# Kernel optimization log

Hardware: AMD Instinct MI355X
Metric: run time of the kernel (lower is better)

The kernel has to match this reference:

```python
import jax, jax.numpy as jnp
import numpy as np

B, N = 2, 512
CS, CZ = 384, 128
H, D, P, PV = 12, 16, 4, 8
W_C = (2.0 / (9.0 * P)) ** 0.5
W_L = (1.0 / 3.0) ** 0.5
CAT = H * CZ + H * D + H * PV * 3 + H * PV  # concat width into output linear


def setup_inputs() -> dict:
    key = jax.random.key(0)
    ks = jax.random.split(key, 14)
    sc = lambda n: np.float32(1.0 / np.sqrt(n))
    s_i = jax.random.normal(ks[0], (B, N, CS), jnp.float32)
    z_ij = jax.random.normal(ks[1], (B, N, N, CZ), jnp.float32)
    rots = jax.random.normal(ks[2], (B, N, 3, 3), jnp.float32)
    trans = jax.random.normal(ks[3], (B, N, 3), jnp.float32)
    wq = jax.random.normal(ks[4], (CS, H, D), jnp.float32) * sc(CS)
    wk = jax.random.normal(ks[5], (CS, H, D), jnp.float32) * sc(CS)
    wv = jax.random.normal(ks[6], (CS, H, D), jnp.float32) * sc(CS)
    wqp = jax.random.normal(ks[7], (CS, H, P, 3), jnp.float32) * sc(CS)
    wkp = jax.random.normal(ks[8], (CS, H, P, 3), jnp.float32) * sc(CS)
    wvp = jax.random.normal(ks[9], (CS, H, PV, 3), jnp.float32) * sc(CS)
    wb = jax.random.normal(ks[10], (CZ, H), jnp.float32) * sc(CZ)
    gamma = jax.random.normal(ks[11], (H,), jnp.float32)
    wout = jax.random.normal(ks[12], (CAT, CS), jnp.float32) * sc(CAT)
    bout = jnp.zeros((CS,), jnp.float32)
    return dict(s_i=s_i, z_ij=z_ij, rots=rots, trans=trans, wq=wq, wk=wk, wv=wv,
                wqp=wqp, wkp=wkp, wvp=wvp, wb=wb, gamma=gamma, wout=wout, bout=bout)


def reference(s_i, z_ij, rots, trans, wq, wk, wv, wqp, wkp, wvp, wb, gamma, wout, bout):
    # rigid apply: x_global = R @ x_local + t, per residue, broadcast over (h, p)
    def rig_apply(x):  # x: (b,i,h,p,3)
        return jnp.einsum('bixy,bihpy->bihpx', rots, x) + trans[:, :, None, None, :]

    def rig_invert_apply(x):  # R^T @ (x - t)
        return jnp.einsum('biyx,bihpy->bihpx', rots, x - trans[:, :, None, None, :])

    q = jnp.einsum('bic,chd->bihd', s_i, wq)
    k = jnp.einsum('bic,chd->bihd', s_i, wk)
    v = jnp.einsum('bic,chd->bihd', s_i, wv)
    qp = jnp.einsum('bic,chpx->bihpx', s_i, wqp)
    kp = jnp.einsum('bic,chpx->bihpx', s_i, wkp)
    vp = jnp.einsum('bic,chpx->bihpx', s_i, wvp)

    b_ij = jnp.einsum('bijc,ch->bijh', z_ij, wb)  # pair bias

    tq = rig_apply(qp)  # (b,i,h,p,3) in global frame
    tk = rig_apply(kp)
    # squared point distances summed over points: (b,i,j,h)
    d2 = jnp.sum((tq[:, :, None] - tk[:, None]) ** 2, axis=(-1, -2))

    a_s = jnp.einsum('bihd,bjhd->bijh', q, k) * np.float32(1.0 / np.sqrt(D))
    logits = W_L * (a_s + b_ij - (W_C * 0.5) * gamma * d2)
    a = jax.nn.softmax(logits, axis=2)  # softmax over j (dim=-2 of bijh)

    o_hat = jnp.einsum('bijh,bijd->bihd', a, z_ij)   # pair-value aggregation
    o = jnp.einsum('bijh,bjhd->bihd', a, v)          # scalar values
    tv = rig_apply(vp)                               # point values in global frame
    o_hp = rig_invert_apply(jnp.einsum('bijh,bjhpx->bihpx', a, tv))
    o_hp_norm = jnp.sqrt(jnp.sum(o_hp ** 2, axis=-1))  # (b,i,h,p)

    cat = jnp.concatenate([
        o_hat.reshape(B, N, H * CZ),
        o.reshape(B, N, H * D),
        o_hp.reshape(B, N, H * PV * 3),
        o_hp_norm.reshape(B, N, H * PV),
    ], axis=-1)
    return cat @ wout + bout
```

## Files before the change

### kernel.cpp

```cpp
#include <hip/hip_runtime.h>
#include <hip/hip_bf16.h>
#include <math.h>

#define BB 2
#define NN 512
#define CS 384
#define CZ 128
#define HH 12
#define CATW 2112

#define W_L_CONST 0.57735026919f
#define W_C_HALF 0.11785113019f
#define INV_SQRT_D 0.25f
#define LGP 516

__global__ void k_proj(const float* __restrict__ s_i,
                       const float* __restrict__ rots,
                       const float* __restrict__ trans,
                       const float* __restrict__ wq,
                       const float* __restrict__ wk,
                       const float* __restrict__ wv,
                       const float* __restrict__ wqp,
                       const float* __restrict__ wkp,
                       const float* __restrict__ wvp,
                       float* __restrict__ qw, float* __restrict__ kw,
                       float* __restrict__ vw, float* __restrict__ tqw,
                       float* __restrict__ tkw, float* __restrict__ tvw) {
  int t0 = blockIdx.x * 2;
  __shared__ float s_row[2][CS];
  __shared__ float praw[2][576];
  __shared__ float R[2][9], T[2][3];
  int tid = threadIdx.x;
  for (int idx = tid; idx < 2 * CS; idx += 256) {
    int tok = idx / CS, c = idx % CS;
    s_row[tok][c] = s_i[(size_t)(t0 + tok) * CS + c];
  }
  if (tid < 18) R[tid / 9][tid % 9] = rots[t0 * 9 + tid];
  if (tid < 6) T[tid / 3][tid % 3] = trans[t0 * 3 + tid];
  __syncthreads();

  for (int f = tid; f < 1152; f += 256) {
    const float* wp;
    int stride;
    if (f < 576) {
      int sel = f / 192, r = f % 192;
      wp = ((sel == 0) ? wq : (sel == 1) ? wk : wv) + r;
      stride = 192;
    } else {
      int g = f - 576;
      if (g < 144)      { wp = wqp + g;        stride = 144; }
      else if (g < 288) { wp = wkp + (g - 144); stride = 144; }
      else              { wp = wvp + (g - 288); stride = 288; }
    }
    float a0 = 0.f, a1 = 0.f;
    #pragma unroll 8
    for (int c = 0; c < CS; c++) {
      float w = wp[(size_t)c * stride];
      a0 += s_row[0][c] * w;
      a1 += s_row[1][c] * w;
    }
    if (f < 576) {
      int sel = f / 192, r = f % 192;
      float* dst = (sel == 0) ? qw : (sel == 1) ? kw : vw;
      dst[(size_t)(t0 + 0) * 192 + r] = a0;
      dst[(size_t)(t0 + 1) * 192 + r] = a1;
    } else {
      int g = f - 576;
      praw[0][g] = a0;
      praw[1][g] = a1;
    }
  }
  __syncthreads();
  for (int idx = tid; idx < 1152; idx += 256) {
    int tok = idx / 576, f = idx % 576;
    int base, r;
    float* dst;
    if (f < 144)      { r = f;       base = 0;   dst = tqw + (size_t)(t0 + tok) * 144; }
    else if (f < 288) { r = f - 144; base = 144; dst = tkw + (size_t)(t0 + tok) * 144; }
    else              { r = f - 288; base = 288; dst = tvw + (size_t)(t0 + tok) * 288; }
    int hp = r / 3, x = r % 3;
    float v0 = praw[tok][base + hp * 3 + 0];
    float v1 = praw[tok][base + hp * 3 + 1];
    float v2 = praw[tok][base + hp * 3 + 2];
    dst[r] = R[tok][x * 3 + 0] * v0 + R[tok][x * 3 + 1] * v1 + R[tok][x * 3 + 2] * v2 + T[tok][x];
  }
}

__global__ void k_bias(const float* __restrict__ z,
                       const float* __restrict__ wb,
                       float* __restrict__ bw) {
  __shared__ float zt[64][129];
  __shared__ float wbs[CZ * HH];
  __shared__ float bbs[64][12];
  int tid = threadIdx.x;
  int r0 = blockIdx.x * 64;
  int bi = r0 >> 9, j0 = r0 & 511;

  for (int idx = tid; idx < CZ * HH; idx += 256) wbs[idx] = wb[idx];
  const float* zbase = z + (size_t)r0 * CZ;
  for (int s = 0; s < 8; s++) {
    int idx = tid + s * 256;
    int row = idx >> 5, q = idx & 31;
    float4 v = *(const float4*)(zbase + (size_t)row * CZ + q * 4);
    zt[row][q * 4 + 0] = v.x;
    zt[row][q * 4 + 1] = v.y;
    zt[row][q * 4 + 2] = v.z;
    zt[row][q * 4 + 3] = v.w;
  }
  __syncthreads();

  int row = tid & 63, hbase = tid >> 6;
  float a0 = 0.f, a1 = 0.f, a2 = 0.f;
  #pragma unroll 8
  for (int c = 0; c < CZ; c++) {
    float zv = zt[row][c];
    a0 += zv * wbs[c * HH + hbase];
    a1 += zv * wbs[c * HH + hbase + 4];
    a2 += zv * wbs[c * HH + hbase + 8];
  }
  bbs[row][hbase] = a0;
  bbs[row][hbase + 4] = a1;
  bbs[row][hbase + 8] = a2;
  __syncthreads();

  for (int idx = tid; idx < 768; idx += 256) {
    int h = idx / 64, jl = idx % 64;
    bw[((size_t)bi * HH + h) * NN + j0 + jl] = bbs[jl][h];
  }
}

__global__ void k_att(const float* __restrict__ z,
                      const float* __restrict__ qw,
                      const float* __restrict__ kw,
                      const float* __restrict__ tqw,
                      const float* __restrict__ tkw,
                      const float* __restrict__ vw,
                      const float* __restrict__ tvw,
                      const float* __restrict__ gamma,
                      const float* __restrict__ rots,
                      const float* __restrict__ trans,
                      const float* __restrict__ bw,
                      float* __restrict__ catm) {
  int bi = blockIdx.x;
  int b = bi / NN;
  __shared__ float lg[HH][LGP];
  __shared__ float opart[4][480];
  __shared__ float qrow[192], tqrow[144], gam[HH];
  __shared__ float rm[HH][4], rs[HH][4];
  __shared__ float praw[288], ohp[288], R[9], T[3];
  int tid = threadIdx.x;
  int lane = tid & 63, wid = tid >> 6;

  const float* bwrow = bw + (size_t)bi * (HH * NN);
  for (int idx = tid; idx < HH * NN; idx += 256)
    lg[idx >> 9][idx & 511] = bwrow[idx];
  for (int idx = tid; idx < 192; idx += 256) qrow[idx] = qw[(size_t)bi * 192 + idx];
  if (tid < 144) tqrow[tid] = tqw[(size_t)bi * 144 + tid];
  if (tid < HH) gam[tid] = gamma[tid];
  if (tid < 9) R[tid] = rots[bi * 9 + tid];
  if (tid < 3) T[tid] = trans[bi * 3 + tid];
  __syncthreads();

  for (int s = 0; s < 24; s++) {
    int task = tid + s * 256;
    int j = task / 12, h = task % 12;
    const float4* kd = (const float4*)(kw + ((size_t)(b * NN + j)) * 192 + h * 16);
    float as = 0.f;
    #pragma unroll
    for (int q = 0; q < 4; q++) {
      float4 kv = kd[q];
      as += qrow[h * 16 + q * 4 + 0] * kv.x + qrow[h * 16 + q * 4 + 1] * kv.y +
            qrow[h * 16 + q * 4 + 2] * kv.z + qrow[h * 16 + q * 4 + 3] * kv.w;
    }
    const float4* td = (const float4*)(tkw + ((size_t)(b * NN + j)) * 144 + h * 12);
    float d2 = 0.f;
    #pragma unroll
    for (int q = 0; q < 3; q++) {
      float4 tv = td[q];
      float d0 = tqrow[h * 12 + q * 4 + 0] - tv.x;
      float d1 = tqrow[h * 12 + q * 4 + 1] - tv.y;
      float d2_ = tqrow[h * 12 + q * 4 + 2] - tv.z;
      float d3 = tqrow[h * 12 + q * 4 + 3] - tv.w;
      d2 += d0 * d0 + d1 * d1 + d2_ * d2_ + d3 * d3;
    }
    lg[h][j] = W_L_CONST * (as * INV_SQRT_D + lg[h][j] - W_C_HALF * gam[h] * d2);
  }
  __syncthreads();

  #pragma unroll
  for (int h = 0; h < HH; h++) {
    float m = fmaxf(lg[h][tid], lg[h][tid + 256]);
    #pragma unroll
    for (int off = 32; off >= 1; off >>= 1) m = fmaxf(m, __shfl_xor(m, off, 64));
    if (lane == 0) rm[h][wid] = m;
  }
  __syncthreads();
  #pragma unroll
  for (int h = 0; h < HH; h++) {
    float mx = fmaxf(fmaxf(rm[h][0], rm[h][1]), fmaxf(rm[h][2], rm[h][3]));
    float e0 = __expf(lg[h][tid] - mx);
    float e1 = __expf(lg[h][tid + 256] - mx);
    lg[h][tid] = e0;
    lg[h][tid + 256] = e1;
    float s = e0 + e1;
    #pragma unroll
    for (int off = 32; off >= 1; off >>= 1) s += __shfl_xor(s, off, 64);
    if (lane == 0) rs[h][wid] = s;
  }
  __syncthreads();
  #pragma unroll
  for (int h = 0; h < HH; h++) {
    float inv = 1.0f / (rs[h][0] + rs[h][1] + rs[h][2] + rs[h][3]);
    lg[h][tid] *= inv;
    lg[h][tid + 256] *= inv;
  }
  __syncthreads();

  float* crow = catm + (size_t)bi * CATW;
  int j0 = wid * 128;

  for (int t = lane; t < 480; t += 64) {
    const float* src;
    int h, str;
    if (t < 192) { h = t >> 4; src = vw + (size_t)b * NN * 192 + t; str = 192; }
    else { int f = t - 192; h = f / 24; src = tvw + (size_t)b * NN * 288 + f; str = 288; }
    float sum = 0.f;
    for (int jj = 0; jj < 128; jj += 4) {
      float4 av = *(const float4*)&lg[h][j0 + jj];
      sum += av.x * src[(size_t)(j0 + jj + 0) * str]
           + av.y * src[(size_t)(j0 + jj + 1) * str]
           + av.z * src[(size_t)(j0 + jj + 2) * str]
           + av.w * src[(size_t)(j0 + jj + 3) * str];
    }
    opart[wid][t] = sum;
  }
  __syncthreads();
  for (int t = tid; t < 480; t += 256) {
    float s = opart[0][t] + opart[1][t] + opart[2][t] + opart[3][t];
    if (t < 192) crow[1536 + t] = s;
    else praw[t - 192] = s;
  }
  __syncthreads();
  for (int f = tid; f < 288; f += 256) {
    int g = f / 3, x = f % 3;
    float v0 = praw[g * 3 + 0] - T[0];
    float v1 = praw[g * 3 + 1] - T[1];
    float v2 = praw[g * 3 + 2] - T[2];
    float val = R[0 * 3 + x] * v0 + R[1 * 3 + x] * v1 + R[2 * 3 + x] * v2;
    ohp[f] = val;
    crow[1728 + f] = val;
  }
  __syncthreads();
  if (tid < 96) {
    float x0 = ohp[tid * 3 + 0];
    float x1 = ohp[tid * 3 + 1];
    float x2 = ohp[tid * 3 + 2];
    crow[2016 + tid] = sqrtf(x0 * x0 + x1 * x1 + x2 * x2);
  }

  int hw = lane >> 5, c4 = (lane & 31) * 4;
  float4 acc[HH];
  #pragma unroll
  for (int h = 0; h < HH; h++) acc[h] = make_float4(0.f, 0.f, 0.f, 0.f);
  for (int stp = 0; stp < 64; stp++) {
    int j = j0 + stp * 2 + hw;
    float4 zv = *(const float4*)(z + ((size_t)bi * NN + j) * CZ + c4);
    #pragma unroll
    for (int h = 0; h < HH; h++) {
      float a = lg[h][j];
      acc[h].x += a * zv.x;
      acc[h].y += a * zv.y;
      acc[h].z += a * zv.z;
      acc[h].w += a * zv.w;
    }
  }
  __syncthreads();
  #pragma unroll
  for (int h = 0; h < HH; h++) {
    acc[h].x += __shfl_xor(acc[h].x, 32, 64);
    acc[h].y += __shfl_xor(acc[h].y, 32, 64);
    acc[h].z += __shfl_xor(acc[h].z, 32, 64);
    acc[h].w += __shfl_xor(acc[h].w, 32, 64);
  }
  float* pbuf = &lg[0][0];
  if (lane < 32) {
    #pragma unroll
    for (int h = 0; h < HH; h++)
      *(float4*)&pbuf[wid * 1536 + h * 128 + lane * 4] = acc[h];
  }
  __syncthreads();
  #pragma unroll
  for (int s = 0; s < 6; s++) {
    int idx = tid + s * 256;
    crow[idx] = pbuf[idx] + pbuf[1536 + idx] + pbuf[3072 + idx] + pbuf[4608 + idx];
  }
}

#define KCH 528
__global__ void k_gemm(const float* __restrict__ catm,
                       const float* __restrict__ wout,
                       float* __restrict__ pout) {
  __shared__ float As[16][68];
  __shared__ float Bs[16][64];
  int tid = threadIdx.x;
  int n0 = blockIdx.x * 64, m0 = blockIdx.y * 64, kbase = blockIdx.z * KCH;
  int tx = tid & 15, ty = tid >> 4;
  int sm = tid & 63, skk4 = tid >> 6;
  int bkk = tid >> 4, bn4 = (tid & 15) * 4;
  float acc[4][4] = {};
  for (int kt = 0; kt < KCH / 16; kt++) {
    int k0 = kbase + kt * 16;
    float4 ga = *(const float4*)(catm + (size_t)(m0 + sm) * CATW + k0 + skk4 * 4);
    float4 gb = *(const float4*)(wout + (size_t)(k0 + bkk) * 384 + n0 + bn4);
    __syncthreads();
    As[skk4 * 4 + 0][sm] = ga.x;
    As[skk4 * 4 + 1][sm] = ga.y;
    As[skk4 * 4 + 2][sm] = ga.z;
    As[skk4 * 4 + 3][sm] = ga.w;
    *(float4*)&Bs[bkk][bn4] = gb;
    __syncthreads();
    #pragma unroll
    for (int kk = 0; kk < 16; kk++) {
      float4 av = *(const float4*)&As[kk][ty * 4];
      float4 bv = *(const float4*)&Bs[kk][tx * 4];
      acc[0][0] += av.x * bv.x; acc[0][1] += av.x * bv.y; acc[0][2] += av.x * bv.z; acc[0][3] += av.x * bv.w;
      acc[1][0] += av.y * bv.x; acc[1][1] += av.y * bv.y; acc[1][2] += av.y * bv.z; acc[1][3] += av.y * bv.w;
      acc[2][0] += av.z * bv.x; acc[2][1] += av.z * bv.y; acc[2][2] += av.z * bv.z; acc[2][3] += av.z * bv.w;
      acc[3][0] += av.w * bv.x; acc[3][1] += av.w * bv.y; acc[3][2] += av.w * bv.z; acc[3][3] += av.w * bv.w;
    }
  }
  float* pdst = pout + (size_t)blockIdx.z * (1024 * 384);
  #pragma unroll
  for (int mm = 0; mm < 4; mm++) {
    *(float4*)&pdst[(size_t)(m0 + ty * 4 + mm) * 384 + n0 + tx * 4] =
        make_float4(acc[mm][0], acc[mm][1], acc[mm][2], acc[mm][3]);
  }
}

__global__ void k_red(const float* __restrict__ pout,
                      const float* __restrict__ bout,
                      float* __restrict__ out) {
  int idx = blockIdx.x * 256 + threadIdx.x;
  const int TOTAL = 1024 * 384;
  float s = pout[idx] + pout[TOTAL + idx] + pout[2 * TOTAL + idx] + pout[3 * TOTAL + idx];
  out[idx] = s + bout[idx % 384];
}

extern "C" void kernel_launch(void* const* d_in, const int* in_sizes, int n_in,
                              void* d_out, int out_size, void* d_ws, size_t ws_size,
                              hipStream_t stream) {
  const float* s_i   = (const float*)d_in[0];
  const float* z     = (const float*)d_in[1];
  const float* rots  = (const float*)d_in[2];
  const float* trans = (const float*)d_in[3];
  const float* wq    = (const float*)d_in[4];
  const float* wk    = (const float*)d_in[5];
  const float* wv    = (const float*)d_in[6];
  const float* wqp   = (const float*)d_in[7];
  const float* wkp   = (const float*)d_in[8];
  const float* wvp   = (const float*)d_in[9];
  const float* wb    = (const float*)d_in[10];
  const float* gamma = (const float*)d_in[11];
  const float* wout  = (const float*)d_in[12];
  const float* bout  = (const float*)d_in[13];
  float* out = (float*)d_out;

  float* ws = (float*)d_ws;
  const size_t TOK = (size_t)BB * NN;
  float* qw  = ws;
  float* kw  = qw + TOK * 192;
  float* vw  = kw + TOK * 192;
  float* tqw = vw + TOK * 192;
  float* tkw = tqw + TOK * 144;
  float* tvw = tkw + TOK * 144;
  float* bw  = tvw + TOK * 288;
  float* catm = bw + TOK * HH * NN;
  float* pout = catm + TOK * CATW;

  k_proj<<<BB * NN / 2, 256, 0, stream>>>(s_i, rots, trans, wq, wk, wv, wqp, wkp, wvp,
                                          qw, kw, vw, tqw, tkw, tvw);
  k_bias<<<BB * NN * NN / 64, 256, 0, stream>>>(z, wb, bw);
  k_att<<<BB * NN, 256, 0, stream>>>(z, qw, kw, tqw, tkw, vw, tvw, gamma, rots, trans,
                                     bw, catm);
  dim3 gg(6, 16, 4);
  k_gemm<<<gg, 256, 0, stream>>>(catm, wout, pout);
  k_red<<<(1024 * 384) / 256, 256, 0, stream>>>(pout, bout, out);
}
```

Baseline: 704.7 us.

## Fuse pair-bias projection into attention with chunked online softmax over z

Removes the separate k_bias kernel and computes the pair bias inside k_att from z tiles staged in shared memory, so z is read from HBM once instead of twice. The attention is restructured into 32-column chunks with an online (running max/sum) softmax, reusing each staged z tile for both the bias and the o_hat aggregation, with the next tile prefetched into registers. This trades a large per-row logits buffer for smaller shared memory and more synchronisation per chunk, plus rescaling work for the accumulators.

```diff
diff --git a/kernel.cpp b/kernel.cpp
--- a/kernel.cpp
+++ b/kernel.cpp
@@ -12,7 +12,11 @@
 #define W_L_CONST 0.57735026919f
 #define W_C_HALF 0.11785113019f
 #define INV_SQRT_D 0.25f
-#define LGP 516
+
+#define CHJ 32
+#define NCH 16
+#define ZSP 132
+#define PCTP 36
 
 __global__ void k_proj(const float* __restrict__ s_i,
                        const float* __restrict__ rots,
@@ -86,195 +90,250 @@
   }
 }
 
-__global__ void k_bias(const float* __restrict__ z,
-                       const float* __restrict__ wb,
-                       float* __restrict__ bw) {
-  __shared__ float zt[64][129];
-  __shared__ float wbs[CZ * HH];
-  __shared__ float bbs[64][12];
-  int tid = threadIdx.x;
-  int r0 = blockIdx.x * 64;
-  int bi = r0 >> 9, j0 = r0 & 511;
-
-  for (int idx = tid; idx < CZ * HH; idx += 256) wbs[idx] = wb[idx];
-  const float* zbase = z + (size_t)r0 * CZ;
-  for (int s = 0; s < 8; s++) {
-    int idx = tid + s * 256;
-    int row = idx >> 5, q = idx & 31;
-    float4 v = *(const float4*)(zbase + (size_t)row * CZ + q * 4);
-    zt[row][q * 4 + 0] = v.x;
-    zt[row][q * 4 + 1] = v.y;
-    zt[row][q * 4 + 2] = v.z;
-    zt[row][q * 4 + 3] = v.w;
-  }
-  __syncthreads();
-
-  int row = tid & 63, hbase = tid >> 6;
-  float a0 = 0.f, a1 = 0.f, a2 = 0.f;
-  #pragma unroll 8
-  for (int c = 0; c < CZ; c++) {
-    float zv = zt[row][c];
-    a0 += zv * wbs[c * HH + hbase];
-    a1 += zv * wbs[c * HH + hbase + 4];
-    a2 += zv * wbs[c * HH + hbase + 8];
-  }
-  bbs[row][hbase] = a0;
-  bbs[row][hbase + 4] = a1;
-  bbs[row][hbase + 8] = a2;
-  __syncthreads();
-
-  for (int idx = tid; idx < 768; idx += 256) {
-    int h = idx / 64, jl = idx % 64;
-    bw[((size_t)bi * HH + h) * NN + j0 + jl] = bbs[jl][h];
-  }
-}
-
-__global__ void k_att(const float* __restrict__ z,
-                      const float* __restrict__ qw,
-                      const float* __restrict__ kw,
-                      const float* __restrict__ tqw,
-                      const float* __restrict__ tkw,
-                      const float* __restrict__ vw,
-                      const float* __restrict__ tvw,
-                      const float* __restrict__ gamma,
-                      const float* __restrict__ rots,
-                      const float* __restrict__ trans,
-                      const float* __restrict__ bw,
-                      float* __restrict__ catm) {
+#define OHACC(hh, pv)                                   \
+  acc[hh].x = fmaf((pv), zv.x, acc[hh].x);              \
+  acc[hh].y = fmaf((pv), zv.y, acc[hh].y);              \
+  acc[hh].z = fmaf((pv), zv.z, acc[hh].z);              \
+  acc[hh].w = fmaf((pv), zv.w, acc[hh].w);
+
+__global__ __launch_bounds__(256, 4) void k_att(
+    const float* __restrict__ z,
+    const float* __restrict__ qw,
+    const float* __restrict__ kw,
+    const float* __restrict__ tqw,
+    const float* __restrict__ tkw,
+    const float* __restrict__ vw,
+    const float* __restrict__ tvw,
+    const float* __restrict__ gamma,
+    const float* __restrict__ rots,
+    const float* __restrict__ trans,
+    const float* __restrict__ wb,
+    float* __restrict__ catm) {
   int bi = blockIdx.x;
-  int b = bi / NN;
-  __shared__ float lg[HH][LGP];
-  __shared__ float opart[4][480];
-  __shared__ float qrow[192], tqrow[144], gam[HH];
-  __shared__ float rm[HH][4], rs[HH][4];
-  __shared__ float praw[288], ohp[288], R[9], T[3];
+  int b = bi >> 9;
   int tid = threadIdx.x;
   int lane = tid & 63, wid = tid >> 6;
 
-  const float* bwrow = bw + (size_t)bi * (HH * NN);
-  for (int idx = tid; idx < HH * NN; idx += 256)
-    lg[idx >> 9][idx & 511] = bwrow[idx];
-  for (int idx = tid; idx < 192; idx += 256) qrow[idx] = qw[(size_t)bi * 192 + idx];
+  __shared__ float pool[6960];
+  float* zs   = pool;
+  float* wbs  = pool + 4224;
+  float* bp   = pool + 5760;
+  float* pcp  = pool + 6144;
+  float* pct  = pool + 6528;
+  float* pbuf = pool;
+  float* praw = pool + 6144;
+  float* ohp  = pool + 6432;
+
+  __shared__ float qrow[192], tqrow[144], gam[HH], Rm[9], Tm[3];
+  __shared__ float mh[HH], sh[HH], fs[HH];
+
+  for (int i = tid; i < CZ * HH; i += 256) wbs[i] = wb[i];
+  for (int i = tid; i < 192; i += 256) qrow[i] = qw[(size_t)bi * 192 + i];
   if (tid < 144) tqrow[tid] = tqw[(size_t)bi * 144 + tid];
-  if (tid < HH) gam[tid] = gamma[tid];
-  if (tid < 9) R[tid] = rots[bi * 9 + tid];
-  if (tid < 3) T[tid] = trans[bi * 3 + tid];
-  __syncthreads();
-
-  for (int s = 0; s < 24; s++) {
-    int task = tid + s * 256;
-    int j = task / 12, h = task % 12;
-    const float4* kd = (const float4*)(kw + ((size_t)(b * NN + j)) * 192 + h * 16);
-    float as = 0.f;
-    #pragma unroll
-    for (int q = 0; q < 4; q++) {
-      float4 kv = kd[q];
-      as += qrow[h * 16 + q * 4 + 0] * kv.x + qrow[h * 16 + q * 4 + 1] * kv.y +
-            qrow[h * 16 + q * 4 + 2] * kv.z + qrow[h * 16 + q * 4 + 3] * kv.w;
-    }
-    const float4* td = (const float4*)(tkw + ((size_t)(b * NN + j)) * 144 + h * 12);
-    float d2 = 0.f;
-    #pragma unroll
-    for (int q = 0; q < 3; q++) {
-      float4 tv = td[q];
-      float d0 = tqrow[h * 12 + q * 4 + 0] - tv.x;
-      float d1 = tqrow[h * 12 + q * 4 + 1] - tv.y;
-      float d2_ = tqrow[h * 12 + q * 4 + 2] - tv.z;
-      float d3 = tqrow[h * 12 + q * 4 + 3] - tv.w;
-      d2 += d0 * d0 + d1 * d1 + d2_ * d2_ + d3 * d3;
-    }
-    lg[h][j] = W_L_CONST * (as * INV_SQRT_D + lg[h][j] - W_C_HALF * gam[h] * d2);
-  }
-  __syncthreads();
-
-  #pragma unroll
-  for (int h = 0; h < HH; h++) {
-    float m = fmaxf(lg[h][tid], lg[h][tid + 256]);
-    #pragma unroll
-    for (int off = 32; off >= 1; off >>= 1) m = fmaxf(m, __shfl_xor(m, off, 64));
-    if (lane == 0) rm[h][wid] = m;
-  }
-  __syncthreads();
-  #pragma unroll
-  for (int h = 0; h < HH; h++) {
-    float mx = fmaxf(fmaxf(rm[h][0], rm[h][1]), fmaxf(rm[h][2], rm[h][3]));
-    float e0 = __expf(lg[h][tid] - mx);
-    float e1 = __expf(lg[h][tid + 256] - mx);
-    lg[h][tid] = e0;
-    lg[h][tid + 256] = e1;
-    float s = e0 + e1;
-    #pragma unroll
-    for (int off = 32; off >= 1; off >>= 1) s += __shfl_xor(s, off, 64);
-    if (lane == 0) rs[h][wid] = s;
-  }
-  __syncthreads();
-  #pragma unroll
-  for (int h = 0; h < HH; h++) {
-    float inv = 1.0f / (rs[h][0] + rs[h][1] + rs[h][2] + rs[h][3]);
-    lg[h][tid] *= inv;
-    lg[h][tid + 256] *= inv;
-  }
-  __syncthreads();
-
-  float* crow = catm + (size_t)bi * CATW;
-  int j0 = wid * 128;
-
-  for (int t = lane; t < 480; t += 64) {
-    const float* src;
-    int h, str;
-    if (t < 192) { h = t >> 4; src = vw + (size_t)b * NN * 192 + t; str = 192; }
-    else { int f = t - 192; h = f / 24; src = tvw + (size_t)b * NN * 288 + f; str = 288; }
-    float sum = 0.f;
-    for (int jj = 0; jj < 128; jj += 4) {
-      float4 av = *(const float4*)&lg[h][j0 + jj];
-      sum += av.x * src[(size_t)(j0 + jj + 0) * str]
-           + av.y * src[(size_t)(j0 + jj + 1) * str]
-           + av.z * src[(size_t)(j0 + jj + 2) * str]
-           + av.w * src[(size_t)(j0 + jj + 3) * str];
-    }
-    opart[wid][t] = sum;
-  }
-  __syncthreads();
-  for (int t = tid; t < 480; t += 256) {
-    float s = opart[0][t] + opart[1][t] + opart[2][t] + opart[3][t];
-    if (t < 192) crow[1536 + t] = s;
-    else praw[t - 192] = s;
-  }
-  __syncthreads();
-  for (int f = tid; f < 288; f += 256) {
-    int g = f / 3, x = f % 3;
-    float v0 = praw[g * 3 + 0] - T[0];
-    float v1 = praw[g * 3 + 1] - T[1];
-    float v2 = praw[g * 3 + 2] - T[2];
-    float val = R[0 * 3 + x] * v0 + R[1 * 3 + x] * v1 + R[2 * 3 + x] * v2;
-    ohp[f] = val;
-    crow[1728 + f] = val;
-  }
-  __syncthreads();
-  if (tid < 96) {
-    float x0 = ohp[tid * 3 + 0];
-    float x1 = ohp[tid * 3 + 1];
-    float x2 = ohp[tid * 3 + 2];
-    crow[2016 + tid] = sqrtf(x0 * x0 + x1 * x1 + x2 * x2);
-  }
-
-  int hw = lane >> 5, c4 = (lane & 31) * 4;
+  if (tid < HH) { gam[tid] = gamma[tid]; mh[tid] = -1e30f; sh[tid] = 0.f; }
+  if (tid < 9) Rm[tid] = rots[bi * 9 + tid];
+  if (tid < 3) Tm[tid] = trans[bi * 3 + tid];
+
+  const float* zrow = z + (size_t)bi * NN * CZ;
+  int jr0 = tid >> 5;
+  int qq = (tid & 31) * 4;
+  {
+    const float* pbz = zrow + qq;
+    *(float4*)&zs[(jr0     ) * ZSP + qq] = *(const float4*)(pbz + (size_t)(jr0     ) * CZ);
+    *(float4*)&zs[(jr0 +  8) * ZSP + qq] = *(const float4*)(pbz + (size_t)(jr0 +  8) * CZ);
+    *(float4*)&zs[(jr0 + 16) * ZSP + qq] = *(const float4*)(pbz + (size_t)(jr0 + 16) * CZ);
+    *(float4*)&zs[(jr0 + 24) * ZSP + qq] = *(const float4*)(pbz + (size_t)(jr0 + 24) * CZ);
+  }
+
+  int jw = wid * 8;
+  int jpar = (wid << 1) | (lane >> 5);
+  int c4 = (lane & 31) * 4;
+  int s0 = tid, s1 = tid + 256;
+  int h0 = (s0 < 192) ? (s0 >> 4) : (s0 - 192) / 24;
+  bool has1 = (s1 < 480);
+  int h1 = has1 ? (s1 - 192) / 24 : 0;
+  float oacc0 = 0.f, oacc1 = 0.f;
+
   float4 acc[HH];
   #pragma unroll
   for (int h = 0; h < HH; h++) acc[h] = make_float4(0.f, 0.f, 0.f, 0.f);
-  for (int stp = 0; stp < 64; stp++) {
-    int j = j0 + stp * 2 + hw;
-    float4 zv = *(const float4*)(z + ((size_t)bi * NN + j) * CZ + c4);
+
+  __syncthreads();
+
+  for (int ch = 0; ch < NCH; ch++) {
+    int jb = ch * CHJ;
+
+    float4 zn0 = make_float4(0, 0, 0, 0), zn1 = zn0, zn2 = zn0, zn3 = zn0;
+    if (ch < NCH - 1) {
+      const float* pbz = zrow + (size_t)(jb + CHJ) * CZ + qq;
+      zn0 = *(const float4*)(pbz + (size_t)(jr0     ) * CZ);
+      zn1 = *(const float4*)(pbz + (size_t)(jr0 +  8) * CZ);
+      zn2 = *(const float4*)(pbz + (size_t)(jr0 + 16) * CZ);
+      zn3 = *(const float4*)(pbz + (size_t)(jr0 + 24) * CZ);
+    }
+
+    {
+      int jsub = lane >> 3, cseg = lane & 7;
+      const float* zr = zs + (jw + jsub) * ZSP + cseg;
+      const float* wr = wbs + cseg * 12;
+      float pb[HH];
+      #pragma unroll
+      for (int h = 0; h < HH; h++) pb[h] = 0.f;
+      #pragma unroll
+      for (int i = 0; i < 16; i++) {
+        float zv = zr[8 * i];
+        float4 w0 = *(const float4*)&wr[96 * i];
+        float4 w1 = *(const float4*)&wr[96 * i + 4];
+        float4 w2 = *(const float4*)&wr[96 * i + 8];
+        pb[0] = fmaf(zv, w0.x, pb[0]);   pb[1] = fmaf(zv, w0.y, pb[1]);
+        pb[2] = fmaf(zv, w0.z, pb[2]);   pb[3] = fmaf(zv, w0.w, pb[3]);
+        pb[4] = fmaf(zv, w1.x, pb[4]);   pb[5] = fmaf(zv, w1.y, pb[5]);
+        pb[6] = fmaf(zv, w1.z, pb[6]);   pb[7] = fmaf(zv, w1.w, pb[7]);
+        pb[8] = fmaf(zv, w2.x, pb[8]);   pb[9] = fmaf(zv, w2.y, pb[9]);
+        pb[10] = fmaf(zv, w2.z, pb[10]); pb[11] = fmaf(zv, w2.w, pb[11]);
+      }
+      #pragma unroll
+      for (int h = 0; h < HH; h++) {
+        pb[h] += __shfl_xor(pb[h], 1, 64);
+        pb[h] += __shfl_xor(pb[h], 2, 64);
+        pb[h] += __shfl_xor(pb[h], 4, 64);
+      }
+      if (cseg == 0) {
+        float* d = bp + (jw + jsub) * 12;
+        *(float4*)&d[0] = make_float4(pb[0], pb[1], pb[2], pb[3]);
+        *(float4*)&d[4] = make_float4(pb[4], pb[5], pb[6], pb[7]);
+        *(float4*)&d[8] = make_float4(pb[8], pb[9], pb[10], pb[11]);
+      }
+    }
+
+    for (int t = lane; t < 96; t += 64) {
+      int jsub2 = t / 12, h = t - jsub2 * 12;
+      int jl = jw + jsub2;
+      size_t grow = (size_t)(b * NN + jb + jl);
+      const float4* kd = (const float4*)(kw + grow * 192 + h * 16);
+      float qk = 0.f;
+      #pragma unroll
+      for (int q = 0; q < 4; q++) {
+        float4 kv = kd[q];
+        qk += qrow[h * 16 + q * 4 + 0] * kv.x + qrow[h * 16 + q * 4 + 1] * kv.y +
+              qrow[h * 16 + q * 4 + 2] * kv.z + qrow[h * 16 + q * 4 + 3] * kv.w;
+      }
+      const float4* td = (const float4*)(tkw + grow * 144 + h * 12);
+      float d2 = 0.f;
+      #pragma unroll
+      for (int q = 0; q < 3; q++) {
+        float4 tv = td[q];
+        float d0 = tqrow[h * 12 + q * 4 + 0] - tv.x;
+        float d1 = tqrow[h * 12 + q * 4 + 1] - tv.y;
+        float dd = tqrow[h * 12 + q * 4 + 2] - tv.z;
+        float d3 = tqrow[h * 12 + q * 4 + 3] - tv.w;
+        d2 += d0 * d0 + d1 * d1 + dd * dd + d3 * d3;
+      }
+      float bias = bp[jl * 12 + h];
+      pcp[jl * 12 + h] =
+          W_L_CONST * (qk * INV_SQRT_D + bias - W_C_HALF * gam[h] * d2);
+    }
+    __syncthreads();
+
+    if (lane < 32) {
+      #pragma unroll
+      for (int hh = 0; hh < 3; hh++) {
+        int h = wid * 3 + hh;
+        float v = pcp[lane * 12 + h];
+        float cm = v;
+        cm = fmaxf(cm, __shfl_xor(cm, 16, 32));
+        cm = fmaxf(cm, __shfl_xor(cm, 8, 32));
+        cm = fmaxf(cm, __shfl_xor(cm, 4, 32));
+        cm = fmaxf(cm, __shfl_xor(cm, 2, 32));
+        cm = fmaxf(cm, __shfl_xor(cm, 1, 32));
+        float mo = mh[h];
+        float nm = fmaxf(mo, cm);
+        float f = __expf(mo - nm);
+        float p = __expf(v - nm);
+        float ps = p;
+        ps += __shfl_xor(ps, 16, 32);
+        ps += __shfl_xor(ps, 8, 32);
+        ps += __shfl_xor(ps, 4, 32);
+        ps += __shfl_xor(ps, 2, 32);
+        ps += __shfl_xor(ps, 1, 32);
+        if (lane == 0) { mh[h] = nm; sh[h] = sh[h] * f + ps; fs[h] = f; }
+        pcp[lane * 12 + h] = p;
+        pct[h * PCTP + lane] = p;
+      }
+    }
+    __syncthreads();
+
     #pragma unroll
     for (int h = 0; h < HH; h++) {
-      float a = lg[h][j];
-      acc[h].x += a * zv.x;
-      acc[h].y += a * zv.y;
-      acc[h].z += a * zv.z;
-      acc[h].w += a * zv.w;
-    }
-  }
-  __syncthreads();
+      float f = fs[h];
+      acc[h].x *= f; acc[h].y *= f; acc[h].z *= f; acc[h].w *= f;
+    }
+    #pragma unroll
+    for (int stp = 0; stp < 4; stp++) {
+      int jl = stp * 8 + jpar;
+      float4 zv = *(const float4*)&zs[jl * ZSP + c4];
+      const float* pr = &pcp[jl * 12];
+      float4 p0 = *(const float4*)&pr[0];
+      float4 p1 = *(const float4*)&pr[4];
+      float4 p2 = *(const float4*)&pr[8];
+      OHACC(0, p0.x)  OHACC(1, p0.y)  OHACC(2, p0.z)  OHACC(3, p0.w)
+      OHACC(4, p1.x)  OHACC(5, p1.y)  OHACC(6, p1.z)  OHACC(7, p1.w)
+      OHACC(8, p2.x)  OHACC(9, p2.y)  OHACC(10, p2.z) OHACC(11, p2.w)
+    }
+
+    {
+      oacc0 *= fs[h0];
+      const float* prr = &pct[h0 * PCTP];
+      if (s0 < 192) {
+        const float* p = vw + ((size_t)(b * NN + jb)) * 192 + s0;
+        #pragma unroll
+        for (int q = 0; q < 8; q++) {
+          float4 pa = *(const float4*)&prr[q * 4];
+          oacc0 = fmaf(pa.x, p[0], oacc0);
+          oacc0 = fmaf(pa.y, p[192], oacc0);
+          oacc0 = fmaf(pa.z, p[384], oacc0);
+          oacc0 = fmaf(pa.w, p[576], oacc0);
+          p += 768;
+        }
+      } else {
+        const float* p = tvw + ((size_t)(b * NN + jb)) * 288 + (s0 - 192);
+        #pragma unroll
+        for (int q = 0; q < 8; q++) {
+          float4 pa = *(const float4*)&prr[q * 4];
+          oacc0 = fmaf(pa.x, p[0], oacc0);
+          oacc0 = fmaf(pa.y, p[288], oacc0);
+          oacc0 = fmaf(pa.z, p[576], oacc0);
+          oacc0 = fmaf(pa.w, p[864], oacc0);
+          p += 1152;
+        }
+      }
+      if (has1) {
+        oacc1 *= fs[h1];
+        const float* prr1 = &pct[h1 * PCTP];
+        const float* p = tvw + ((size_t)(b * NN + jb)) * 288 + (s1 - 192);
+        #pragma unroll
+        for (int q = 0; q < 8; q++) {
+          float4 pa = *(const float4*)&prr1[q * 4];
+          oacc1 = fmaf(pa.x, p[0], oacc1);
+          oacc1 = fmaf(pa.y, p[288], oacc1);
+          oacc1 = fmaf(pa.z, p[576], oacc1);
+          oacc1 = fmaf(pa.w, p[864], oacc1);
+          p += 1152;
+        }
+      }
+    }
+    __syncthreads();
+
+    if (ch < NCH - 1) {
+      *(float4*)&zs[(jr0     ) * ZSP + qq] = zn0;
+      *(float4*)&zs[(jr0 +  8) * ZSP + qq] = zn1;
+      *(float4*)&zs[(jr0 + 16) * ZSP + qq] = zn2;
+      *(float4*)&zs[(jr0 + 24) * ZSP + qq] = zn3;
+      __syncthreads();
+    }
+  }
+
+  if (tid < HH) fs[tid] = 1.0f / sh[tid];
   #pragma unroll
   for (int h = 0; h < HH; h++) {
     acc[h].x += __shfl_xor(acc[h].x, 32, 64);
@@ -282,17 +341,43 @@
     acc[h].z += __shfl_xor(acc[h].z, 32, 64);
     acc[h].w += __shfl_xor(acc[h].w, 32, 64);
   }
-  float* pbuf = &lg[0][0];
+  __syncthreads();
+
+  float* crow = catm + (size_t)bi * CATW;
   if (lane < 32) {
     #pragma unroll
     for (int h = 0; h < HH; h++)
       *(float4*)&pbuf[wid * 1536 + h * 128 + lane * 4] = acc[h];
   }
-  __syncthreads();
+  {
+    float ov0 = oacc0 * fs[h0];
+    if (s0 < 192) crow[1536 + s0] = ov0;
+    else praw[s0 - 192] = ov0;
+    if (has1) praw[s1 - 192] = oacc1 * fs[h1];
+  }
+  __syncthreads();
+
   #pragma unroll
   for (int s = 0; s < 6; s++) {
-    int idx = tid + s * 256;
-    crow[idx] = pbuf[idx] + pbuf[1536 + idx] + pbuf[3072 + idx] + pbuf[4608 + idx];
+    int u = tid + s * 256;
+    crow[u] = (pbuf[u] + pbuf[1536 + u] + pbuf[3072 + u] + pbuf[4608 + u]) *
+              fs[u >> 7];
+  }
+  for (int f = tid; f < 288; f += 256) {
+    int g = f / 3, x = f - g * 3;
+    float v0 = praw[g * 3 + 0] - Tm[0];
+    float v1 = praw[g * 3 + 1] - Tm[1];
+    float v2 = praw[g * 3 + 2] - Tm[2];
+    float val = Rm[0 * 3 + x] * v0 + Rm[1 * 3 + x] * v1 + Rm[2 * 3 + x] * v2;
+    ohp[f] = val;
+    crow[1728 + f] = val;
+  }
+  __syncthreads();
+  if (tid < 96) {
+    float x0 = ohp[tid * 3 + 0];
+    float x1 = ohp[tid * 3 + 1];
+    float x2 = ohp[tid * 3 + 2];
+    crow[2016 + tid] = sqrtf(x0 * x0 + x1 * x1 + x2 * x2);
   }
 }
 
@@ -379,9 +464,8 @@
 
   k_proj<<<BB * NN / 2, 256, 0, stream>>>(s_i, rots, trans, wq, wk, wv, wqp, wkp, wvp,
                                           qw, kw, vw, tqw, tkw, tvw);
-  k_bias<<<BB * NN * NN / 64, 256, 0, stream>>>(z, wb, bw);
   k_att<<<BB * NN, 256, 0, stream>>>(z, qw, kw, tqw, tkw, vw, tvw, gamma, rots, trans,
-                                     bw, catm);
+                                     wb, catm);
   dim3 gg(6, 16, 4);
   k_gemm<<<gg, 256, 0, stream>>>(catm, wout, pout);
   k_red<<<(1024 * 384) / 256, 256, 0, stream>>>(pout, bout, out);
```

New measurement: 1.177 ms. +67.0%, slower.

## Restructure pair-bias kernel with XOR-swizzled LDS, float4 reads and 2 rows per thread

Applied to the files above, without the earlier changes.

The pair-bias projection kernel now handles 128 rows per block instead of 64. The z tile is stored in shared memory with an XOR swizzle so it can be written and read as float4 without bank conflicts. wb is transposed into shared memory, and each thread computes 3 heads for 2 rows using vectorized shared-memory loads. The aim is fewer LDS instructions and less bank-conflict overhead in a kernel that streams the whole 256 MB z tensor. The cost is 64 KB of shared memory per block, which can lower occupancy.

```diff
diff --git a/kernel.cpp b/kernel.cpp
--- a/kernel.cpp
+++ b/kernel.cpp
@@ -86,45 +86,69 @@
   }
 }
 
+#define BR 128
 __global__ void k_bias(const float* __restrict__ z,
                        const float* __restrict__ wb,
                        float* __restrict__ bw) {
-  __shared__ float zt[64][129];
-  __shared__ float wbs[CZ * HH];
-  __shared__ float bbs[64][12];
+  __shared__ float zt[BR * 128];
+  __shared__ float wbt[12][128];
+  __shared__ float bbs[BR][13];
   int tid = threadIdx.x;
-  int r0 = blockIdx.x * 64;
+  int r0 = blockIdx.x * BR;
   int bi = r0 >> 9, j0 = r0 & 511;
 
-  for (int idx = tid; idx < CZ * HH; idx += 256) wbs[idx] = wb[idx];
+  for (int idx = tid; idx < CZ * HH; idx += 256) {
+    int h = idx >> 7, c = idx & 127;
+    wbt[h][c] = wb[c * HH + h];
+  }
   const float* zbase = z + (size_t)r0 * CZ;
-  for (int s = 0; s < 8; s++) {
+  #pragma unroll
+  for (int s = 0; s < 16; s++) {
     int idx = tid + s * 256;
-    int row = idx >> 5, q = idx & 31;
-    float4 v = *(const float4*)(zbase + (size_t)row * CZ + q * 4);
-    zt[row][q * 4 + 0] = v.x;
-    zt[row][q * 4 + 1] = v.y;
-    zt[row][q * 4 + 2] = v.z;
-    zt[row][q * 4 + 3] = v.w;
-  }
-  __syncthreads();
-
-  int row = tid & 63, hbase = tid >> 6;
-  float a0 = 0.f, a1 = 0.f, a2 = 0.f;
+    int row = idx >> 5, c4 = idx & 31;
+    float4 v = *(const float4*)(zbase + (size_t)row * CZ + c4 * 4);
+    *(float4*)&zt[row * 128 + ((c4 ^ (row & 7)) << 2)] = v;
+  }
+  __syncthreads();
+
+  int lane = tid & 63, wid = tid >> 6;
+  int hb = wid * 3;
+  int rA = lane, rB = lane + 64;
+  int sA = rA & 7, sB = rB & 7;
+  const float* w0 = wbt[hb + 0];
+  const float* w1 = wbt[hb + 1];
+  const float* w2 = wbt[hb + 2];
+  const float* zArow = &zt[rA * 128];
+  const float* zBrow = &zt[rB * 128];
+  float aA0 = 0.f, aA1 = 0.f, aA2 = 0.f, aB0 = 0.f, aB1 = 0.f, aB2 = 0.f;
   #pragma unroll 8
-  for (int c = 0; c < CZ; c++) {
-    float zv = zt[row][c];
-    a0 += zv * wbs[c * HH + hbase];
-    a1 += zv * wbs[c * HH + hbase + 4];
-    a2 += zv * wbs[c * HH + hbase + 8];
-  }
-  bbs[row][hbase] = a0;
-  bbs[row][hbase + 4] = a1;
-  bbs[row][hbase + 8] = a2;
-  __syncthreads();
-
-  for (int idx = tid; idx < 768; idx += 256) {
-    int h = idx / 64, jl = idx % 64;
+  for (int c4 = 0; c4 < 32; c4++) {
+    float4 zA = *(const float4*)&zArow[(c4 ^ sA) << 2];
+    float4 zB = *(const float4*)&zBrow[(c4 ^ sB) << 2];
+    float4 v0 = *(const float4*)&w0[c4 << 2];
+    float4 v1 = *(const float4*)&w1[c4 << 2];
+    float4 v2 = *(const float4*)&w2[c4 << 2];
+    aA0 = fmaf(zA.x, v0.x, aA0); aA0 = fmaf(zA.y, v0.y, aA0);
+    aA0 = fmaf(zA.z, v0.z, aA0); aA0 = fmaf(zA.w, v0.w, aA0);
+    aA1 = fmaf(zA.x, v1.x, aA1); aA1 = fmaf(zA.y, v1.y, aA1);
+    aA1 = fmaf(zA.z, v1.z, aA1); aA1 = fmaf(zA.w, v1.w, aA1);
+    aA2 = fmaf(zA.x, v2.x, aA2); aA2 = fmaf(zA.y, v2.y, aA2);
+    aA2 = fmaf(zA.z, v2.z, aA2); aA2 = fmaf(zA.w, v2.w, aA2);
+    aB0 = fmaf(zB.x, v0.x, aB0); aB0 = fmaf(zB.y, v0.y, aB0);
+    aB0 = fmaf(zB.z, v0.z, aB0); aB0 = fmaf(zB.w, v0.w, aB0);
+    aB1 = fmaf(zB.x, v1.x, aB1); aB1 = fmaf(zB.y, v1.y, aB1);
+    aB1 = fmaf(zB.z, v1.z, aB1); aB1 = fmaf(zB.w, v1.w, aB1);
+    aB2 = fmaf(zB.x, v2.x, aB2); aB2 = fmaf(zB.y, v2.y, aB2);
+    aB2 = fmaf(zB.z, v2.z, aB2); aB2 = fmaf(zB.w, v2.w, aB2);
+  }
+  bbs[rA][hb + 0] = aA0; bbs[rA][hb + 1] = aA1; bbs[rA][hb + 2] = aA2;
+  bbs[rB][hb + 0] = aB0; bbs[rB][hb + 1] = aB1; bbs[rB][hb + 2] = aB2;
+  __syncthreads();
+
+  #pragma unroll
+  for (int s = 0; s < 6; s++) {
+    int idx = tid + s * 256;
+    int h = idx >> 7, jl = idx & 127;
     bw[((size_t)bi * HH + h) * NN + j0 + jl] = bbs[jl][h];
   }
 }
@@ -379,7 +403,7 @@
 
   k_proj<<<BB * NN / 2, 256, 0, stream>>>(s_i, rots, trans, wq, wk, wv, wqp, wkp, wvp,
                                           qw, kw, vw, tqw, tkw, tvw);
-  k_bias<<<BB * NN * NN / 64, 256, 0, stream>>>(z, wb, bw);
+  k_bias<<<BB * NN * NN / BR, 256, 0, stream>>>(z, wb, bw);
   k_att<<<BB * NN, 256, 0, stream>>>(z, qw, kw, tqw, tkw, vw, tvw, gamma, rots, trans,
                                      bw, catm);
   dim3 gg(6, 16, 4);
```

Result: slower. 757.2 us (+7.4%).

## Register-tile projection and pair-bias kernels, drop shared-memory staging in bias

Applied to the files above, without the earlier changes.

The pair-bias kernel now keeps a 16x3 slice of the bias weights in registers for each lane. Each lane streams 16 channels of two z rows with float4 loads, and a 3-step xor-shuffle sums partial results across 8 lanes. The shared-memory transpose and both block barriers are gone, and each block covers 256 rows instead of 64. The projection kernel is unrolled so each thread holds five output features with float4 reads of the token rows. In exchange, half the threads in the fifth slot redundantly recompute the same features. Both kernels also get waves-per-EU hints to steer register allocation.

```diff
diff --git a/kernel.cpp b/kernel.cpp
--- a/kernel.cpp
+++ b/kernel.cpp
@@ -14,18 +14,19 @@
 #define INV_SQRT_D 0.25f
 #define LGP 516
 
-__global__ void k_proj(const float* __restrict__ s_i,
-                       const float* __restrict__ rots,
-                       const float* __restrict__ trans,
-                       const float* __restrict__ wq,
-                       const float* __restrict__ wk,
-                       const float* __restrict__ wv,
-                       const float* __restrict__ wqp,
-                       const float* __restrict__ wkp,
-                       const float* __restrict__ wvp,
-                       float* __restrict__ qw, float* __restrict__ kw,
-                       float* __restrict__ vw, float* __restrict__ tqw,
-                       float* __restrict__ tkw, float* __restrict__ tvw) {
+__global__ __attribute__((amdgpu_waves_per_eu(2, 4)))
+void k_proj(const float* __restrict__ s_i,
+            const float* __restrict__ rots,
+            const float* __restrict__ trans,
+            const float* __restrict__ wq,
+            const float* __restrict__ wk,
+            const float* __restrict__ wv,
+            const float* __restrict__ wqp,
+            const float* __restrict__ wkp,
+            const float* __restrict__ wvp,
+            float* __restrict__ qw, float* __restrict__ kw,
+            float* __restrict__ vw, float* __restrict__ tqw,
+            float* __restrict__ tkw, float* __restrict__ tvw) {
   int t0 = blockIdx.x * 2;
   __shared__ float s_row[2][CS];
   __shared__ float praw[2][576];
@@ -39,35 +40,62 @@
   if (tid < 6) T[tid / 3][tid % 3] = trans[t0 * 3 + tid];
   __syncthreads();
 
-  for (int f = tid; f < 1152; f += 256) {
-    const float* wp;
-    int stride;
+  int fa[5];
+  fa[0] = tid; fa[1] = tid + 256; fa[2] = tid + 512; fa[3] = tid + 768;
+  fa[4] = 1024 + (tid & 127);
+  const float* wp[5];
+  int st[5];
+  #pragma unroll
+  for (int t = 0; t < 5; t++) {
+    int f = fa[t];
     if (f < 576) {
       int sel = f / 192, r = f % 192;
-      wp = ((sel == 0) ? wq : (sel == 1) ? wk : wv) + r;
-      stride = 192;
+      wp[t] = ((sel == 0) ? wq : (sel == 1) ? wk : wv) + r;
+      st[t] = 192;
     } else {
       int g = f - 576;
-      if (g < 144)      { wp = wqp + g;        stride = 144; }
-      else if (g < 288) { wp = wkp + (g - 144); stride = 144; }
-      else              { wp = wvp + (g - 288); stride = 288; }
-    }
-    float a0 = 0.f, a1 = 0.f;
-    #pragma unroll 8
-    for (int c = 0; c < CS; c++) {
-      float w = wp[(size_t)c * stride];
-      a0 += s_row[0][c] * w;
-      a1 += s_row[1][c] * w;
-    }
+      if (g < 144)      { wp[t] = wqp + g;         st[t] = 144; }
+      else if (g < 288) { wp[t] = wkp + (g - 144); st[t] = 144; }
+      else              { wp[t] = wvp + (g - 288); st[t] = 288; }
+    }
+  }
+  float acc[5][2];
+  #pragma unroll
+  for (int t = 0; t < 5; t++) { acc[t][0] = 0.f; acc[t][1] = 0.f; }
+
+  for (int c4 = 0; c4 < 96; c4++) {
+    float4 s0 = *(const float4*)&s_row[0][c4 * 4];
+    float4 s1 = *(const float4*)&s_row[1][c4 * 4];
+    #pragma unroll
+    for (int t = 0; t < 5; t++) {
+      const float* p = wp[t] + (size_t)(c4 * 4) * st[t];
+      float w0 = p[0];
+      float w1 = p[st[t]];
+      float w2 = p[2 * st[t]];
+      float w3 = p[3 * st[t]];
+      acc[t][0] = fmaf(s0.x, w0, acc[t][0]);
+      acc[t][0] = fmaf(s0.y, w1, acc[t][0]);
+      acc[t][0] = fmaf(s0.z, w2, acc[t][0]);
+      acc[t][0] = fmaf(s0.w, w3, acc[t][0]);
+      acc[t][1] = fmaf(s1.x, w0, acc[t][1]);
+      acc[t][1] = fmaf(s1.y, w1, acc[t][1]);
+      acc[t][1] = fmaf(s1.z, w2, acc[t][1]);
+      acc[t][1] = fmaf(s1.w, w3, acc[t][1]);
+    }
+  }
+
+  #pragma unroll
+  for (int t = 0; t < 5; t++) {
+    int f = fa[t];
     if (f < 576) {
       int sel = f / 192, r = f % 192;
       float* dst = (sel == 0) ? qw : (sel == 1) ? kw : vw;
-      dst[(size_t)(t0 + 0) * 192 + r] = a0;
-      dst[(size_t)(t0 + 1) * 192 + r] = a1;
+      dst[(size_t)(t0 + 0) * 192 + r] = acc[t][0];
+      dst[(size_t)(t0 + 1) * 192 + r] = acc[t][1];
     } else {
       int g = f - 576;
-      praw[0][g] = a0;
-      praw[1][g] = a1;
+      praw[0][g] = acc[t][0];
+      praw[1][g] = acc[t][1];
     }
   }
   __syncthreads();
@@ -86,46 +114,73 @@
   }
 }
 
-__global__ void k_bias(const float* __restrict__ z,
-                       const float* __restrict__ wb,
-                       float* __restrict__ bw) {
-  __shared__ float zt[64][129];
-  __shared__ float wbs[CZ * HH];
-  __shared__ float bbs[64][12];
+#define BQ(v, q, sx0, sx1, sx2)                                        \
+  sx0 = fmaf(v.x, w[(q)*4 + 0][0], sx0);                               \
+  sx1 = fmaf(v.x, w[(q)*4 + 0][1], sx1);                               \
+  sx2 = fmaf(v.x, w[(q)*4 + 0][2], sx2);                               \
+  sx0 = fmaf(v.y, w[(q)*4 + 1][0], sx0);                               \
+  sx1 = fmaf(v.y, w[(q)*4 + 1][1], sx1);                               \
+  sx2 = fmaf(v.y, w[(q)*4 + 1][2], sx2);                               \
+  sx0 = fmaf(v.z, w[(q)*4 + 2][0], sx0);                               \
+  sx1 = fmaf(v.z, w[(q)*4 + 2][1], sx1);                               \
+  sx2 = fmaf(v.z, w[(q)*4 + 2][2], sx2);                               \
+  sx0 = fmaf(v.w, w[(q)*4 + 3][0], sx0);                               \
+  sx1 = fmaf(v.w, w[(q)*4 + 3][1], sx1);                               \
+  sx2 = fmaf(v.w, w[(q)*4 + 3][2], sx2);
+
+__global__ __attribute__((amdgpu_waves_per_eu(2, 4)))
+void k_bias(const float* __restrict__ z,
+            const float* __restrict__ wb,
+            float* __restrict__ bw) {
   int tid = threadIdx.x;
-  int r0 = blockIdx.x * 64;
-  int bi = r0 >> 9, j0 = r0 & 511;
-
-  for (int idx = tid; idx < CZ * HH; idx += 256) wbs[idx] = wb[idx];
-  const float* zbase = z + (size_t)r0 * CZ;
-  for (int s = 0; s < 8; s++) {
-    int idx = tid + s * 256;
-    int row = idx >> 5, q = idx & 31;
-    float4 v = *(const float4*)(zbase + (size_t)row * CZ + q * 4);
-    zt[row][q * 4 + 0] = v.x;
-    zt[row][q * 4 + 1] = v.y;
-    zt[row][q * 4 + 2] = v.z;
-    zt[row][q * 4 + 3] = v.w;
-  }
-  __syncthreads();
-
-  int row = tid & 63, hbase = tid >> 6;
-  float a0 = 0.f, a1 = 0.f, a2 = 0.f;
-  #pragma unroll 8
-  for (int c = 0; c < CZ; c++) {
-    float zv = zt[row][c];
-    a0 += zv * wbs[c * HH + hbase];
-    a1 += zv * wbs[c * HH + hbase + 4];
-    a2 += zv * wbs[c * HH + hbase + 8];
-  }
-  bbs[row][hbase] = a0;
-  bbs[row][hbase + 4] = a1;
-  bbs[row][hbase + 8] = a2;
-  __syncthreads();
-
-  for (int idx = tid; idx < 768; idx += 256) {
-    int h = idx / 64, jl = idx % 64;
-    bw[((size_t)bi * HH + h) * NN + j0 + jl] = bbs[jl][h];
+  int l32 = tid & 31;
+  int grp = tid >> 5;
+  int hg = l32 >> 3;
+  int cs = l32 & 7;
+
+  float w[16][3];
+  #pragma unroll
+  for (int cc = 0; cc < 16; cc++) {
+    const float* p = wb + (size_t)(cs * 16 + cc) * HH + hg * 3;
+    w[cc][0] = p[0]; w[cc][1] = p[1]; w[cc][2] = p[2];
+  }
+
+  int r0 = blockIdx.x * 256 + grp * 32;
+  int bi = r0 >> 9;
+  for (int rr = 0; rr < 32; rr += 2) {
+    const float* zA = z + (size_t)(r0 + rr) * CZ + cs * 16;
+    const float* zB = zA + CZ;
+    float4 a0 = ((const float4*)zA)[0];
+    float4 a1 = ((const float4*)zA)[1];
+    float4 a2 = ((const float4*)zA)[2];
+    float4 a3 = ((const float4*)zA)[3];
+    float4 b0 = ((const float4*)zB)[0];
+    float4 b1 = ((const float4*)zB)[1];
+    float4 b2 = ((const float4*)zB)[2];
+    float4 b3 = ((const float4*)zB)[3];
+    float sA0 = 0.f, sA1 = 0.f, sA2 = 0.f;
+    float sB0 = 0.f, sB1 = 0.f, sB2 = 0.f;
+    BQ(a0, 0, sA0, sA1, sA2)
+    BQ(a1, 1, sA0, sA1, sA2)
+    BQ(a2, 2, sA0, sA1, sA2)
+    BQ(a3, 3, sA0, sA1, sA2)
+    BQ(b0, 0, sB0, sB1, sB2)
+    BQ(b1, 1, sB0, sB1, sB2)
+    BQ(b2, 2, sB0, sB1, sB2)
+    BQ(b3, 3, sB0, sB1, sB2)
+    sA0 += __shfl_xor(sA0, 1, 64); sA0 += __shfl_xor(sA0, 2, 64); sA0 += __shfl_xor(sA0, 4, 64);
+    sA1 += __shfl_xor(sA1, 1, 64); sA1 += __shfl_xor(sA1, 2, 64); sA1 += __shfl_xor(sA1, 4, 64);
+    sA2 += __shfl_xor(sA2, 1, 64); sA2 += __shfl_xor(sA2, 2, 64); sA2 += __shfl_xor(sA2, 4, 64);
+    sB0 += __shfl_xor(sB0, 1, 64); sB0 += __shfl_xor(sB0, 2, 64); sB0 += __shfl_xor(sB0, 4, 64);
+    sB1 += __shfl_xor(sB1, 1, 64); sB1 += __shfl_xor(sB1, 2, 64); sB1 += __shfl_xor(sB1, 4, 64);
+    sB2 += __shfl_xor(sB2, 1, 64); sB2 += __shfl_xor(sB2, 2, 64); sB2 += __shfl_xor(sB2, 4, 64);
+    if (cs == 0) {
+      int jA = (r0 + rr) & 511;
+      float* d = bw + ((size_t)bi * HH + hg * 3) * NN + jA;
+      *(float2*)&d[0]      = make_float2(sA0, sB0);
+      *(float2*)&d[NN]     = make_float2(sA1, sB1);
+      *(float2*)&d[2 * NN] = make_float2(sA2, sB2);
+    }
   }
 }
 
@@ -379,7 +434,7 @@
 
   k_proj<<<BB * NN / 2, 256, 0, stream>>>(s_i, rots, trans, wq, wk, wv, wqp, wkp, wvp,
                                           qw, kw, vw, tqw, tkw, tvw);
-  k_bias<<<BB * NN * NN / 64, 256, 0, stream>>>(z, wb, bw);
+  k_bias<<<BB * NN * NN / 256, 256, 0, stream>>>(z, wb, bw);
   k_att<<<BB * NN, 256, 0, stream>>>(z, qw, kw, tqw, tkw, vw, tvw, gamma, rots, trans,
                                      bw, catm);
   dim3 gg(6, 16, 4);
```

After: 953.0 us. 35.2% more time.
